# Kernel tuning notes

Measured on AMD Instinct MI355X. Metric: run time of the kernel, lower is better.

The kernel has to match this reference:

```python
import jax, jax.numpy as jnp
import numpy as np

BS = 16384      # batch of tree nodes
N_CH = 8        # children per node (= max_output_degree)
H = 256         # h_size
RANK = 16       # tensor-train rank
N_AGGR = 4      # parallel aggregators
T = 64          # t_size (type embedding dim)
SCALE = 0.05    # param init scale (keeps the length-8 matmul chain stable)


def setup_inputs() -> dict:
    key = jax.random.key(0)
    ks = jax.random.split(key, 8)
    R = (RANK + 1) * RANK
    return {
        "neighbour_h": jax.random.normal(ks[0], (BS, N_CH, H), jnp.float32),
        "type_embs": jax.random.normal(ks[1], (BS, T), jnp.float32),
        "U": jax.random.normal(ks[2], (N_CH, N_AGGR, H, R), jnp.float32) * SCALE,
        "b": jax.random.normal(ks[3], (N_CH, N_AGGR, 1, R), jnp.float32) * SCALE,
        "U_type": jax.random.normal(ks[4], (N_AGGR, T, RANK), jnp.float32) * SCALE,
        "b_type": jax.random.normal(ks[5], (N_AGGR, 1, RANK), jnp.float32) * SCALE,
        "U_output": jax.random.normal(ks[6], (N_AGGR, RANK, H), jnp.float32) * SCALE,
        "b_output": jax.random.normal(ks[7], (N_AGGR, 1, H), jnp.float32) * SCALE,
    }


def reference(neighbour_h, type_embs, U, b, U_type, b_type, U_output, b_output):
    bs, n_ch, h = neighbour_h.shape
    n_aggr, _, rank = U_type.shape

    # per-child projection to TT cores: [bs, n_ch, n_aggr, (rank+1)*rank]
    ris = jnp.einsum('bch,cahr->bcar', neighbour_h, U[:n_ch]) + b[:n_ch, :, 0, :]
    ris = ris.reshape(bs, n_ch, n_aggr, rank + 1, rank)

    # initial rank vector from type embeddings: [bs, n_aggr, rank]
    rank_ris0 = jnp.einsum('bt,atr->bar', type_embs, U_type) + b_type[:, 0, :]

    # sequential TT chain over children (loop-carried dependency) via scan
    xs = jnp.moveaxis(ris, 1, 0)  # [n_ch, bs, n_aggr, rank+1, rank]

    def step(carry, aux):
        U_rank = aux[:, :, :-1, :]   # [bs, n_aggr, rank, rank]
        b_rank = aux[:, :, -2, :]    # row -2 (matches torch's aux[:,:,-2:-1,:])
        return jnp.einsum('bar,barq->baq', carry, U_rank) + b_rank, None

    rank_ris, _ = jax.lax.scan(step, rank_ris0, xs)

    # output projection: [bs, n_aggr, h]
    out = jnp.einsum('bar,arh->bah', rank_ris, U_output) + b_output[:, 0, :]
    return out.reshape(bs, n_aggr * h)
```

## Files before the change

kernel.cpp:

```cpp
#include <hip/hip_runtime.h>


#define N_CH   8
#define H_DIM  256
#define R_FULL 272

typedef __bf16 bf16x8 __attribute__((ext_vector_type(8)));
typedef float  f32x4  __attribute__((ext_vector_type(4)));

union BF8 {
  bf16x8 v;
  unsigned short s[8];
  uint4 q;
};

typedef __attribute__((address_space(3))) unsigned int       lds_u32;
typedef __attribute__((address_space(1))) const unsigned int glb_u32;

static __device__ __forceinline__ unsigned short f2bf(float x) {
  union { float f; unsigned int u; } t; t.f = x;
  unsigned int u = t.u;
  return (unsigned short)((u + 0x7FFFu + ((u >> 16) & 1u)) >> 16);
}
static __device__ __forceinline__ unsigned int pk2(float a, float b) {
  return (unsigned int)f2bf(a) | ((unsigned int)f2bf(b) << 16);
}
static __device__ __forceinline__ void ll16(const void* g, void* l) {
  __builtin_amdgcn_global_load_lds((glb_u32*)g, (lds_u32*)l, 16, 0, 0);
}

__global__ void prep_U_kernel(const float* __restrict__ U, unsigned int* __restrict__ Ubf) {
  unsigned int idx  = blockIdx.x * 256u + threadIdx.x;
  unsigned int jp   = idx & 3u;
  unsigned int lane = (idx >> 2) & 63u;
  unsigned int ks   = (idx >> 8) & 7u;
  unsigned int t    = (idx >> 11) & 15u;
  unsigned int ca   = idx >> 15;
  unsigned int h = ks * 32u + (lane >> 4) * 8u + jp * 2u;
  unsigned int r = t * 16u + (lane & 15u);
  const float* src = U + ((size_t)ca * 256u + h) * R_FULL + r;
  Ubf[idx] = pk2(src[0], src[R_FULL]);
}

#define SM_A  0
#define SM_B0 32768
#define SM_B1 65536

__global__ __launch_bounds__(1024)
void tt_main(const float* __restrict__ nh,
             const float* __restrict__ ty,
             const char*  __restrict__ Ubf,
             const float* __restrict__ bB,
             const float* __restrict__ Ut,
             const float* __restrict__ bt,
             const float* __restrict__ Uo,
             const float* __restrict__ bo,
             float* __restrict__ out)
{
  extern __shared__ char smem[];
  const int tid  = threadIdx.x;
  const int lane = tid & 63;
  const int w    = tid >> 6;
  const int a    = w & 3;
  const int sg   = w >> 2;
  const int b0   = blockIdx.x * 64;
  const int row0 = b0 + sg * 16;
  const int lr   = lane & 15;
  const int lg   = lane >> 4;

  f32x4 carry;
  {
    float btv = bt[a * 16 + lr];
    f32x4 acc = { btv, btv, btv, btv };
#pragma unroll
    for (int ks = 0; ks < 2; ++ks) {
      BF8 utf, af;
#pragma unroll
      for (int j = 0; j < 8; ++j) {
        utf.s[j] = f2bf(Ut[a * 1024 + (ks * 32 + lg * 8 + j) * 16 + lr]);
        af.s[j]  = f2bf(ty[(size_t)(row0 + lr) * 64 + ks * 32 + lg * 8 + j]);
      }
      acc = __builtin_amdgcn_mfma_f32_16x16x32_bf16(af.v, utf.v, acc, 0, 0, 0);
    }
    carry = acc;
  }

  auto issueB = [&](int c, int t, int bufoff) {
#pragma unroll
    for (int q = 0; q < 2; ++q) {
      const int ch = w * 2 + q;
      const char* g = Ubf + (((((size_t)c * 4 + (ch >> 3)) * 16 + t) * 8 + (ch & 7)) << 10)
                          + lane * 16;
      ll16(g, smem + bufoff + ch * 1024);
    }
  };

#pragma unroll 1
  for (int c = 0; c < N_CH; ++c) {
    {
      const int sg_s = tid >> 8;
      const int ksh  = (tid >> 6) & 3;
      const int ln   = tid & 63;
      const int row  = sg_s * 16 + (ln & 15);
#pragma unroll
      for (int p = 0; p < 2; ++p) {
        const int ks = ksh * 2 + p;
        const int k0 = ks * 32 + (ln >> 4) * 8;
        const float* s = nh + ((size_t)(b0 + row) * N_CH + c) * H_DIM + k0;
        float4 x0 = *(const float4*)s;
        float4 x1 = *(const float4*)(s + 4);
        uint4 qv;
        qv.x = pk2(x0.x, x0.y); qv.y = pk2(x0.z, x0.w);
        qv.z = pk2(x1.x, x1.y); qv.w = pk2(x1.z, x1.w);
        *(uint4*)(smem + SM_A + ((sg_s * 8 + ks) * 64 + ln) * 16) = qv;
      }
    }
    issueB(c, 0, SM_B0);
    __syncthreads();

    BF8 Af[8];
#pragma unroll
    for (int ks = 0; ks < 8; ++ks)
      Af[ks].q = *(const uint4*)(smem + SM_A + ((sg * 8 + ks) * 64 + lane) * 16);

    const float* bBp = bB + (c * 4 + a) * R_FULL;
    float bb[16];
#pragma unroll
    for (int t = 0; t < 16; ++t) bb[t] = bBp[t * 16 + lr];

    f32x4 partial = { 0.f, 0.f, 0.f, 0.f };

#pragma unroll 1
    for (int t = 0; t < 16; ++t) {
      if (t < 15) issueB(c, t + 1, (t & 1) ? SM_B0 : SM_B1);
      const int bufoff = (t & 1) ? SM_B1 : SM_B0;
      float bias = bb[t];
      f32x4 acc = { bias, bias, bias, bias };
      uint4 Bq[8];
#pragma unroll
      for (int ks = 0; ks < 8; ++ks)
        Bq[ks] = *(const uint4*)(smem + bufoff + (a * 8 + ks) * 1024 + lane * 16);
#pragma unroll
      for (int ks = 0; ks < 8; ++ks) {
        BF8 bf; bf.q = Bq[ks];
        acc = __builtin_amdgcn_mfma_f32_16x16x32_bf16(Af[ks].v, bf.v, acc, 0, 0, 0);
      }
      const float extra = (t == 15) ? 1.0f : 0.0f;
      const int   srcl  = (lane & 48) | t;
#pragma unroll
      for (int i = 0; i < 4; ++i) {
        float cv = __shfl(carry[i], srcl, 64) + extra;
        partial[i] += cv * acc[i];
      }
      __syncthreads();
    }
    carry = partial;
  }

  float uo[4][16], bov[4];
#pragma unroll
  for (int chk = 0; chk < 4; ++chk) {
    bov[chk] = bo[a * 256 + chk * 64 + lane];
#pragma unroll
    for (int r = 0; r < 16; ++r)
      uo[chk][r] = Uo[(size_t)a * 4096 + r * 256 + chk * 64 + lane];
  }
#pragma unroll
  for (int g = 0; g < 4; ++g)
#pragma unroll
    for (int i = 0; i < 4; ++i) {
      const int m = g * 4 + i;
      float cv[16];
#pragma unroll
      for (int r = 0; r < 16; ++r) cv[r] = __shfl(carry[i], (g << 4) | r, 64);
#pragma unroll
      for (int chk = 0; chk < 4; ++chk) {
        float v = bov[chk];
#pragma unroll
        for (int r = 0; r < 16; ++r) v += cv[r] * uo[chk][r];
        out[(size_t)(row0 + m) * 1024 + a * 256 + chk * 64 + lane] = v;
      }
    }
}

extern "C" void kernel_launch(void* const* d_in, const int* in_sizes, int n_in,
                              void* d_out, int out_size, void* d_ws, size_t ws_size,
                              hipStream_t stream) {
  const float* nh = (const float*)d_in[0];
  const float* ty = (const float*)d_in[1];
  const float* U  = (const float*)d_in[2];
  const float* bB = (const float*)d_in[3];
  const float* Ut = (const float*)d_in[4];
  const float* bt = (const float*)d_in[5];
  const float* Uo = (const float*)d_in[6];
  const float* bo = (const float*)d_in[7];
  float* out = (float*)d_out;

  unsigned int* Ubf32 = (unsigned int*)d_ws;

  prep_U_kernel<<<4096, 256, 0, stream>>>(U, Ubf32);

  static int smem_set = 0;
  (void)hipFuncSetAttribute((const void*)tt_main,
                            hipFuncAttributeMaxDynamicSharedMemorySize, 98304);
  (void)smem_set;
  tt_main<<<256, 1024, 98304, stream>>>(nh, ty, (const char*)d_ws,
                                        bB, Ut, bt, Uo, bo, out);
}
```

Before: 369.8 us.

## Triple-buffer weight tiles across child boundaries with vmcnt-based barriers

Replaces the double-buffered per-child B-tile pipeline with a three-slot ring. The ring prefetches two tiles ahead over a flattened child×tile index, so loads keep flowing across child boundaries instead of restarting at each child. The full __syncthreads per tile becomes an explicit s_waitcnt vmcnt(2) plus a raw s_barrier, the tile loop is fully unrolled, and MFMA blocks are wrapped in s_setprio. This raises LDS use to 128 KB and relies on hand-managed wait counts, which could break if the compiler reorders or adds global loads.

```diff
diff --git a/kernel.cpp b/kernel.cpp
--- a/kernel.cpp
+++ b/kernel.cpp
@@ -42,9 +42,8 @@
   Ubf[idx] = pk2(src[0], src[R_FULL]);
 }
 
-#define SM_A  0
-#define SM_B0 32768
-#define SM_B1 65536
+#define SM_A    0
+#define SM_B(k) (32768 + (k) * 32768)
 
 __global__ __launch_bounds__(1024)
 void tt_main(const float* __restrict__ nh,
@@ -85,66 +84,82 @@
     carry = acc;
   }
 
-  auto issueB = [&](int c, int t, int bufoff) {
+  auto issueB = [&](int g) {
+    const int cB  = g >> 4;
+    const int tB  = g & 15;
+    const int bo_ = SM_B(g % 3);
 #pragma unroll
     for (int q = 0; q < 2; ++q) {
       const int ch = w * 2 + q;
-      const char* g = Ubf + (((((size_t)c * 4 + (ch >> 3)) * 16 + t) * 8 + (ch & 7)) << 10)
-                          + lane * 16;
-      ll16(g, smem + bufoff + ch * 1024);
+      const char* gp = Ubf + (((((size_t)cB * 4 + (ch >> 3)) * 16 + tB) * 8 + (ch & 7)) << 10)
+                           + lane * 16;
+      ll16(gp, smem + bo_ + ch * 1024);
     }
   };
+
+  issueB(0);
+  issueB(1);
+
+  BF8   Af[8];
+  float bb[16];
+  f32x4 partial;
 
 #pragma unroll 1
   for (int c = 0; c < N_CH; ++c) {
-    {
-      const int sg_s = tid >> 8;
-      const int ksh  = (tid >> 6) & 3;
-      const int ln   = tid & 63;
-      const int row  = sg_s * 16 + (ln & 15);
-#pragma unroll
-      for (int p = 0; p < 2; ++p) {
-        const int ks = ksh * 2 + p;
-        const int k0 = ks * 32 + (ln >> 4) * 8;
-        const float* s = nh + ((size_t)(b0 + row) * N_CH + c) * H_DIM + k0;
-        float4 x0 = *(const float4*)s;
-        float4 x1 = *(const float4*)(s + 4);
-        uint4 qv;
-        qv.x = pk2(x0.x, x0.y); qv.y = pk2(x0.z, x0.w);
-        qv.z = pk2(x1.x, x1.y); qv.w = pk2(x1.z, x1.w);
-        *(uint4*)(smem + SM_A + ((sg_s * 8 + ks) * 64 + ln) * 16) = qv;
-      }
-    }
-    issueB(c, 0, SM_B0);
-    __syncthreads();
-
-    BF8 Af[8];
-#pragma unroll
-    for (int ks = 0; ks < 8; ++ks)
-      Af[ks].q = *(const uint4*)(smem + SM_A + ((sg * 8 + ks) * 64 + lane) * 16);
-
-    const float* bBp = bB + (c * 4 + a) * R_FULL;
-    float bb[16];
-#pragma unroll
-    for (int t = 0; t < 16; ++t) bb[t] = bBp[t * 16 + lr];
-
-    f32x4 partial = { 0.f, 0.f, 0.f, 0.f };
-
-#pragma unroll 1
+#pragma unroll
     for (int t = 0; t < 16; ++t) {
-      if (t < 15) issueB(c, t + 1, (t & 1) ? SM_B0 : SM_B1);
-      const int bufoff = (t & 1) ? SM_B1 : SM_B0;
-      float bias = bb[t];
-      f32x4 acc = { bias, bias, bias, bias };
+      const int g = c * 16 + t;
+
+      if (t == 15 && c == N_CH - 1) asm volatile("s_waitcnt vmcnt(0)");
+      else                          asm volatile("s_waitcnt vmcnt(2)");
+      __builtin_amdgcn_s_barrier();
+
+      if (t == 0) {
+        {
+          const int sg_s = tid >> 8;
+          const int ksh  = (tid >> 6) & 3;
+          const int ln   = tid & 63;
+          const int row  = sg_s * 16 + (ln & 15);
+#pragma unroll
+          for (int p = 0; p < 2; ++p) {
+            const int ks = ksh * 2 + p;
+            const int k0 = ks * 32 + (ln >> 4) * 8;
+            const float* s = nh + ((size_t)(b0 + row) * N_CH + c) * H_DIM + k0;
+            float4 x0 = *(const float4*)s;
+            float4 x1 = *(const float4*)(s + 4);
+            uint4 qv;
+            qv.x = pk2(x0.x, x0.y); qv.y = pk2(x0.z, x0.w);
+            qv.z = pk2(x1.x, x1.y); qv.w = pk2(x1.z, x1.w);
+            *(uint4*)(smem + SM_A + ((sg_s * 8 + ks) * 64 + ln) * 16) = qv;
+          }
+        }
+        asm volatile("s_waitcnt lgkmcnt(0)");
+        __builtin_amdgcn_s_barrier();
+#pragma unroll
+        for (int ks = 0; ks < 8; ++ks)
+          Af[ks].q = *(const uint4*)(smem + SM_A + ((sg * 8 + ks) * 64 + lane) * 16);
+        const float* bBp = bB + (c * 4 + a) * R_FULL;
+#pragma unroll
+        for (int t2 = 0; t2 < 16; ++t2) bb[t2] = bBp[t2 * 16 + lr];
+        partial[0] = partial[1] = partial[2] = partial[3] = 0.f;
+      }
+
+      if (g + 2 < N_CH * 16) issueB(g + 2);
+
+      const int bufoff = SM_B((c + t) % 3);
+      f32x4 acc = { bb[t], bb[t], bb[t], bb[t] };
       uint4 Bq[8];
 #pragma unroll
       for (int ks = 0; ks < 8; ++ks)
         Bq[ks] = *(const uint4*)(smem + bufoff + (a * 8 + ks) * 1024 + lane * 16);
+      __builtin_amdgcn_s_setprio(1);
 #pragma unroll
       for (int ks = 0; ks < 8; ++ks) {
         BF8 bf; bf.q = Bq[ks];
         acc = __builtin_amdgcn_mfma_f32_16x16x32_bf16(Af[ks].v, bf.v, acc, 0, 0, 0);
       }
+      __builtin_amdgcn_s_setprio(0);
+
       const float extra = (t == 15) ? 1.0f : 0.0f;
       const int   srcl  = (lane & 48) | t;
 #pragma unroll
@@ -152,7 +167,6 @@
         float cv = __shfl(carry[i], srcl, 64) + extra;
         partial[i] += cv * acc[i];
       }
-      __syncthreads();
     }
     carry = partial;
   }
@@ -166,13 +180,13 @@
       uo[chk][r] = Uo[(size_t)a * 4096 + r * 256 + chk * 64 + lane];
   }
 #pragma unroll
-  for (int g = 0; g < 4; ++g)
+  for (int gq = 0; gq < 4; ++gq)
 #pragma unroll
     for (int i = 0; i < 4; ++i) {
-      const int m = g * 4 + i;
+      const int m = gq * 4 + i;
       float cv[16];
 #pragma unroll
-      for (int r = 0; r < 16; ++r) cv[r] = __shfl(carry[i], (g << 4) | r, 64);
+      for (int r = 0; r < 16; ++r) cv[r] = __shfl(carry[i], (gq << 4) | r, 64);
 #pragma unroll
       for (int chk = 0; chk < 4; ++chk) {
         float v = bov[chk];
@@ -200,10 +214,8 @@
 
   prep_U_kernel<<<4096, 256, 0, stream>>>(U, Ubf32);
 
-  static int smem_set = 0;
   (void)hipFuncSetAttribute((const void*)tt_main,
-                            hipFuncAttributeMaxDynamicSharedMemorySize, 98304);
-  (void)smem_set;
-  tt_main<<<256, 1024, 98304, stream>>>(nh, ty, (const char*)d_ws,
-                                        bB, Ut, bt, Uo, bo, out);
-}
+                            hipFuncAttributeMaxDynamicSharedMemorySize, 131072);
+  tt_main<<<256, 1024, 131072, stream>>>(nh, ty, (const char*)d_ws,
+                                         bB, Ut, bt, Uo, bo, out);
+}
```

Result: slower. 503.7 us (+36.2%).
